# Performance work log

Hardware: AMD Instinct MI355X
Metric: run time of the kernel (lower is better)

Reference implementation:

```python
import jax, jax.numpy as jnp
import numpy as np


def _rotate_half(x):
    x1, x2 = jnp.split(x, 2, axis=-1)
    return jnp.concatenate((-x2, x1), axis=-1)


def setup_inputs() -> dict:
    key = jax.random.key(0)
    ks = jax.random.split(key, 8)
    B, T, C, H = 2, 2048, 1024, 16
    Dh = C // H
    x = jax.random.normal(ks[0], (B, T, C), dtype=jnp.float32)
    # RoPE tables (T, head_dim)
    inv_freq = 1.0 / (10000.0 ** (np.arange(0, Dh, 2, dtype=np.float32) / Dh))
    pos = np.arange(T, dtype=np.float32)
    freqs = np.einsum('t,f->tf', pos, inv_freq)
    emb = np.concatenate([freqs, freqs], axis=-1)
    cos = jnp.asarray(np.cos(emb), dtype=jnp.float32)
    sin = jnp.asarray(np.sin(emb), dtype=jnp.float32)
    # causal mask: 1 where attending allowed, 0 elsewhere
    mask = jnp.tril(jnp.ones((T, T), dtype=jnp.int32))
    s = 0.02
    Wq = jax.random.normal(ks[1], (C, C), dtype=jnp.float32) * s
    Wk = jax.random.normal(ks[2], (C, C), dtype=jnp.float32) * s
    Wv = jax.random.normal(ks[3], (C, C), dtype=jnp.float32) * s
    Wo = jax.random.normal(ks[4], (C, C), dtype=jnp.float32) * s
    return {"x": x, "cos": cos, "sin": sin, "mask": mask, "n_heads": H,
            "Wq": Wq, "Wk": Wk, "Wv": Wv, "Wo": Wo}


def reference(x, cos, sin, mask, n_heads, Wq, Wk, Wv, Wo):
    B, T, C = x.shape
    H = n_heads
    Dh = C // H
    scale = Dh ** (-0.5)
    # projections (torch Linear: x @ W.T), reshape to (B, H, T, Dh)
    def proj(W):
        return (x @ W.T).reshape(B, T, H, Dh).transpose(0, 2, 1, 3)
    q, k, v = proj(Wq), proj(Wk), proj(Wv)
    # RoPE: cos/sin broadcast as (1, 1, T, Dh)
    c = cos[None, None]
    s = sin[None, None]
    q = q * c + _rotate_half(q) * s
    k = k * c + _rotate_half(k) * s
    att = jnp.einsum('bhtd,bhsd->bhts', q, k) * scale
    att = jnp.where(mask == 0, -jnp.inf, att)
    att = jax.nn.softmax(att, axis=-1)
    out = jnp.einsum('bhts,bhsd->bhtd', att, v)
    out = out.transpose(0, 2, 1, 3).reshape(B, T, C)
    return out @ Wo.T
```

## Files before the change

kernel.cpp:

```cpp
#include <hip/hip_runtime.h>
#include <stdint.h>

#define B_   2
#define T_   2048
#define C_   1024
#define H_   16
#define BT   4096
#define KDIM 1024

typedef unsigned short u16;
typedef __attribute__((ext_vector_type(8))) __bf16 bf16v8;
typedef __attribute__((ext_vector_type(4))) float f32x4;
typedef __attribute__((ext_vector_type(16))) float f32x16;
typedef __attribute__((ext_vector_type(4))) unsigned int u32x4;
typedef __attribute__((ext_vector_type(2))) unsigned int u32x2;

#define MFMA16(a, b, c) __builtin_amdgcn_mfma_f32_16x16x32_bf16((a), (b), (c), 0, 0, 0)
#define MFMA32(a, b, c) __builtin_amdgcn_mfma_f32_32x32x16_bf16((a), (b), (c), 0, 0, 0)

#define BARRIER() do { asm volatile("" ::: "memory"); \
                       __builtin_amdgcn_s_barrier();  \
                       asm volatile("" ::: "memory"); } while (0)

__device__ __forceinline__ u16 f2bf(float f) {
  __bf16 h = (__bf16)f;
  union { __bf16 h; u16 u; } v; v.h = h;
  return v.u;
}
__device__ __forceinline__ float bf2f(u16 u) {
  union { uint32_t u; float f; } v; v.u = (uint32_t)u << 16;
  return v.f;
}

__device__ __forceinline__ void xhalf(uint32_t a, uint32_t b,
                                      uint32_t& lo, uint32_t& hi) {
#if defined(__has_builtin) && __has_builtin(__builtin_amdgcn_permlane32_swap)
  u32x2 r = __builtin_amdgcn_permlane32_swap(a, b, false, false);
  lo = r.x; hi = r.y;
#else
  const bool upper = (threadIdx.x & 32) != 0;
  lo = upper ? __shfl_xor(b, 32) : a;
  hi = upper ? b : __shfl_xor(a, 32);
#endif
}

__device__ __forceinline__ void gload16(const void* g, void* l) {
  __builtin_amdgcn_global_load_lds((__attribute__((address_space(1))) void*)g,
                                   (__attribute__((address_space(3))) void*)l,
                                   16, 0, 0);
}

__global__ __launch_bounds__(256) void cvt_f32_bf16(const float* __restrict__ in,
                                                    u16* __restrict__ out, int n) {
  int i = (blockIdx.x * 256 + threadIdx.x) * 4;
  if (i + 3 < n) {
    float4 v = *(const float4*)(in + i);
    ushort4 o;
    o.x = f2bf(v.x); o.y = f2bf(v.y); o.z = f2bf(v.z); o.w = f2bf(v.w);
    *(ushort4*)(out + i) = o;
  }
}

__global__ __launch_bounds__(256) void cvt_weights(
    const float* __restrict__ wq, const float* __restrict__ wk,
    const float* __restrict__ wv, const float* __restrict__ wo,
    u16* __restrict__ qkv_dst, u16* __restrict__ o_dst) {
  const int bid = blockIdx.x;
  const int sel = bid >> 10;
  const float* src = (sel == 0) ? wq : (sel == 1) ? wk : (sel == 2) ? wv : wo;
  u16* dst = (sel < 3) ? (qkv_dst + sel * 1048576) : o_dst;
  const int i = ((bid & 1023) * 256 + threadIdx.x) * 4;
  float4 v = *(const float4*)(src + i);
  ushort4 o;
  o.x = f2bf(v.x); o.y = f2bf(v.y); o.z = f2bf(v.z); o.w = f2bf(v.w);
  *(ushort4*)(dst + i) = o;
}

template<int EPI, int NN>
__global__ __launch_bounds__(256, 2) void gemm128(
    const u16* __restrict__ A, const u16* __restrict__ Bm,
    float* __restrict__ Cf,
    u16* __restrict__ qo, u16* __restrict__ ko, u16* __restrict__ vt,
    const float* __restrict__ cosT, const float* __restrict__ sinT)
{
  __shared__ __align__(16) u16 As[2][128 * 64];
  __shared__ __align__(16) u16 Bs[2][128 * 64];
  const int tid = threadIdx.x;
  const int lane = tid & 63;
  const int w = tid >> 6;
  const int wm = w >> 1, wn = w & 1;
  const int lmod = lane & 15, ldiv = lane >> 4;

  constexpr int NBX = NN / 128;
  constexpr int XG_BY = (NBX == 24) ? 8 : 4;
  constexpr int XG_BX = (NBX == 24) ? 12 : 8;
  const int x = blockIdx.x & 7;
  const int i = blockIdx.x >> 3;
  const int gy = (NBX == 24) ? (x >> 1) : x;
  const int gx = (NBX == 24) ? (x & 1) : 0;
  const int by = gy * XG_BY + (i % XG_BY);
  const int bx = gx * XG_BX + (i / XG_BY);
  const int row0 = by * 128, col0 = bx * 128;

  const int srow = tid >> 3;
  const int sswz = ((tid & 7) * 16) ^ ((srow & 7) << 4);
  const char* Abase = (const char*)A + (size_t)(row0 + srow) * (KDIM * 2) + sswz;
  const char* Bbase = (const char*)Bm + (size_t)(col0 + srow) * (KDIM * 2) + sswz;
  const int ldst = (tid & 192) * 16;

  auto stage = [&](int buf, int t) {
    const int kb = t * 128;
#pragma unroll
    for (int c = 0; c < 4; ++c)
      gload16(Abase + (size_t)c * 32 * (KDIM * 2) + kb,
              (char*)As[buf] + c * 4096 + ldst);
#pragma unroll
    for (int c = 0; c < 4; ++c)
      gload16(Bbase + (size_t)c * 32 * (KDIM * 2) + kb,
              (char*)Bs[buf] + c * 4096 + ldst);
  };

  f32x4 acc[4][4] = {};
  stage(0, 0);

  for (int t = 0; t < KDIM / 64; ++t) {
    const int cur = t & 1;
    BARRIER();
    if (t + 1 < KDIM / 64) {
      stage(cur ^ 1, t + 1);
      asm volatile("s_waitcnt vmcnt(8)" ::: "memory");
    } else {
      asm volatile("s_waitcnt vmcnt(0)" ::: "memory");
    }
    BARRIER();

    bf16v8 af[4][2], bfr[4][2];
#pragma unroll
    for (int mf = 0; mf < 4; ++mf) {
      const int rr = wm * 64 + mf * 16 + lmod;
#pragma unroll
      for (int kc = 0; kc < 2; ++kc)
        af[mf][kc] = *(const bf16v8*)((const char*)As[cur] + rr * 128 +
                          ((kc * 64 + ldiv * 16) ^ ((rr & 7) << 4)));
    }
#pragma unroll
    for (int nf = 0; nf < 4; ++nf) {
      const int rr = wn * 64 + nf * 16 + lmod;
#pragma unroll
      for (int kc = 0; kc < 2; ++kc)
        bfr[nf][kc] = *(const bf16v8*)((const char*)Bs[cur] + rr * 128 +
                          ((kc * 64 + ldiv * 16) ^ ((rr & 7) << 4)));
    }
#pragma unroll
    for (int kc = 0; kc < 2; ++kc)
#pragma unroll
      for (int mf = 0; mf < 4; ++mf)
#pragma unroll
        for (int nf = 0; nf < 4; ++nf)
          acc[mf][nf] = MFMA16(af[mf][kc], bfr[nf][kc], acc[mf][nf]);
  }

  if (EPI == 0) {
#pragma unroll
    for (int mf = 0; mf < 4; ++mf) {
      const int mbase = row0 + wm * 64 + mf * 16 + ldiv * 4;
#pragma unroll
      for (int nf = 0; nf < 4; ++nf) {
        const int n = col0 + wn * 64 + nf * 16 + lmod;
#pragma unroll
        for (int r = 0; r < 4; ++r)
          Cf[(size_t)(mbase + r) * NN + n] = acc[mf][nf][r];
      }
    }
  } else {
    const int nb = col0 + wn * 64;
    const int proj = nb >> 10;
    const int hh = (nb & 1023) >> 6;
    if (proj < 2) {
      u16* dst = proj ? ko : qo;
#pragma unroll
      for (int mf = 0; mf < 4; ++mf) {
#pragma unroll
        for (int r = 0; r < 4; ++r) {
          const int m = row0 + wm * 64 + mf * 16 + ldiv * 4 + r;
          const int b = m >> 11, t = m & 2047;
          u16* drow = dst + ((size_t)(b * H_ + hh) * T_ + t) * 64;
#pragma unroll
          for (int nf = 0; nf < 4; ++nf) {
            const int d = nf * 16 + lmod;
            const float cs = cosT[t * 64 + d];
            const float sn = sinT[t * 64 + d];
            const float other = (nf < 2) ? acc[mf][nf + 2][r] : acc[mf][nf - 2][r];
            float val = (nf < 2) ? (acc[mf][nf][r] * cs - other * sn)
                                 : (acc[mf][nf][r] * cs + other * sn);
            if (proj == 0) val *= 0.18033688011112042f;
            drow[d] = f2bf(val);
          }
        }
      }
    } else {
      BARRIER();
      char* scr = (char*)As + w * 8192;
#pragma unroll
      for (int nf = 0; nf < 4; ++nf)
#pragma unroll
        for (int mf = 0; mf < 4; ++mf)
#pragma unroll
          for (int rp = 0; rp < 2; ++rp) {
            const int dd = nf * 16 + lmod;
            const int t0 = mf * 16 + ldiv * 4 + rp * 2;
            const uint32_t pk = (uint32_t)f2bf(acc[mf][nf][rp * 2]) |
                                ((uint32_t)f2bf(acc[mf][nf][rp * 2 + 1]) << 16);
            *(uint32_t*)(scr + ((dd * 128 + t0 * 2) ^ ((dd & 7) << 4))) = pk;
          }
      __syncthreads();
      const int trow = row0 + wm * 64;
      const int bb = trow >> 11, tl = trow & 2047;
#pragma unroll
      for (int j = 0; j < 8; ++j) {
        const int dd = j * 8 + (lane >> 3);
        const int c = lane & 7;
        const u32x4 vv = *(const u32x4*)(scr + ((dd * 128 + c * 16) ^ ((dd & 7) << 4)));
        u16* drow = vt + ((size_t)((bb * H_ + hh) * 64 + dd)) * T_ + tl;
        *(u32x4*)((char*)drow + c * 16) = vv;
      }
    }
  }
}

__global__ __launch_bounds__(256, 2) void attn_fwd4(
    const u16* __restrict__ Q, const u16* __restrict__ K,
    const u16* __restrict__ Vt, u16* __restrict__ O,
    u16* __restrict__ part_o, float* __restrict__ pml)
{
  __shared__ __align__(16) u16 Kl[2][64 * 64];
  __shared__ __align__(16) u16 Vl[2][64 * 64];
  const int xcd = blockIdx.x & 7;
  const int i   = blockIdx.x >> 3;
  const int bh  = xcd * 4 + (i & 3);
  const int r   = i >> 2;
  int qb0, t0, t1, sid;
  if (r < 8) {
    qb0 = r * 128; t0 = 0; t1 = 2 * r + 2; sid = -1;
  } else {
    const int s = r - 8;
    const int c = 8 + (s >> 1);
    const int half = s & 1;
    qb0 = c * 128;
    t0 = half * (c + 1); t1 = t0 + (c + 1);
    sid = (bh * 8 + (c - 8)) * 2 + half;
  }

  const int tid = threadIdx.x, lane = tid & 63, w = tid >> 6;
  const int l31 = lane & 31, hi = lane >> 5;
  const int qrow = qb0 + w * 32;

  bf16v8 qf[4];
  {
    const u16* qp = Q + ((size_t)bh * T_ + qrow + l31) * 64 + hi * 8;
    qf[0] = *(const bf16v8*)(qp);
    qf[1] = *(const bf16v8*)(qp + 16);
    qf[2] = *(const bf16v8*)(qp + 32);
    qf[3] = *(const bf16v8*)(qp + 48);
  }

  float m2 = -1e30f, lsum = 0.f;
  f32x16 oacc0 = {}, oacc1 = {};

  const int scolb = (tid & 7) * 16;
  const int ldst = (tid & 192) * 16;

  auto stage = [&](int buf, int t) {
    const int s0 = t << 6;
#pragma unroll
    for (int c = 0; c < 2; ++c) {
      const int row = (c * 256 + tid) >> 3;
      const int sw = scolb ^ ((row & 7) << 4);
      gload16((const char*)(K + ((size_t)bh * T_ + s0 + row) * 64) + sw,
              (char*)Kl[buf] + c * 4096 + ldst);
    }
#pragma unroll
    for (int c = 0; c < 2; ++c) {
      const int row = (c * 256 + tid) >> 3;
      const int sw = scolb ^ ((row & 7) << 4);
      gload16((const char*)(Vt + ((size_t)(bh * 64 + row)) * T_ + s0) + sw,
              (char*)Vl[buf] + c * 4096 + ldst);
    }
  };

  auto substep = [&](int cur, int sub, int s0_sub) {
    bf16v8 kf[4], vf[4];
#pragma unroll
    for (int c = 0; c < 4; ++c) {
      const int row = sub * 32 + l31;
      kf[c] = *(const bf16v8*)((const char*)Kl[cur] + row * 128 +
                  ((c * 32 + hi * 16) ^ ((row & 7) << 4)));
    }
#pragma unroll
    for (int db = 0; db < 2; ++db)
#pragma unroll
      for (int kg = 0; kg < 2; ++kg) {
        const int row = db * 32 + l31;
        vf[db * 2 + kg] = *(const bf16v8*)((const char*)Vl[cur] + row * 128 +
                  ((sub * 64 + kg * 32 + hi * 16) ^ ((row & 7) << 4)));
      }
    f32x16 s = {};
    s = MFMA32(kf[0], qf[0], s);
    s = MFMA32(kf[1], qf[1], s);
    s = MFMA32(kf[2], qf[2], s);
    s = MFMA32(kf[3], qf[3], s);
    if (s0_sub + 31 > qrow) {
#pragma unroll
      for (int r2 = 0; r2 < 16; ++r2) {
        const int key = s0_sub + (r2 & 3) + 8 * (r2 >> 2) + 4 * hi;
        if (key > qrow + l31) s[r2] = -1e30f;
      }
    }
    float t8[8];
#pragma unroll
    for (int r2 = 0; r2 < 8; ++r2) t8[r2] = fmaxf(s[r2], s[r2 + 8]);
    float t4a = fmaxf(t8[0], t8[4]), t4b = fmaxf(t8[1], t8[5]);
    float t4c = fmaxf(t8[2], t8[6]), t4d = fmaxf(t8[3], t8[7]);
    float pmax = fmaxf(fmaxf(t4a, t4b), fmaxf(t4c, t4d));
    {
      uint32_t lo, hh2;
      xhalf(__builtin_bit_cast(uint32_t, pmax), __builtin_bit_cast(uint32_t, pmax), lo, hh2);
      pmax = fmaxf(__builtin_bit_cast(float, lo), __builtin_bit_cast(float, hh2));
    }
    if (!__all(pmax <= m2 + 11.5416f)) {
      const float mnew = fmaxf(m2, pmax);
      const float rs = __builtin_amdgcn_exp2f(m2 - mnew);
      lsum *= rs;
#pragma unroll
      for (int r2 = 0; r2 < 16; ++r2) { oacc0[r2] *= rs; oacc1[r2] *= rs; }
      m2 = mnew;
    }
    float p[16];
#pragma unroll
    for (int r2 = 0; r2 < 16; ++r2) p[r2] = __builtin_amdgcn_exp2f(s[r2] - m2);
    float a8[8];
#pragma unroll
    for (int r2 = 0; r2 < 8; ++r2) a8[r2] = p[r2] + p[r2 + 8];
    float a4a = a8[0] + a8[4], a4b = a8[1] + a8[5];
    float a4c = a8[2] + a8[6], a4d = a8[3] + a8[7];
    float ts = (a4a + a4b) + (a4c + a4d);
    {
      uint32_t lo, hh2;
      xhalf(__builtin_bit_cast(uint32_t, ts), __builtin_bit_cast(uint32_t, ts), lo, hh2);
      ts = __builtin_bit_cast(float, lo) + __builtin_bit_cast(float, hh2);
    }
    lsum += ts;
    uint32_t o[8];
#pragma unroll
    for (int jj = 0; jj < 8; ++jj) {
      const int r0 = 4 * (jj >> 1) + 2 * (jj & 1);
      uint32_t d;
      asm("v_cvt_pk_bf16_f32 %0, %1, %2" : "=v"(d) : "v"(p[r0]), "v"(p[r0 + 1]));
      o[jj] = d;
    }
#pragma unroll
    for (int kg = 0; kg < 2; ++kg) {
      uint32_t f0, f1, f2, f3;
      xhalf(o[4 * kg + 0], o[4 * kg + 2], f0, f2);
      xhalf(o[4 * kg + 1], o[4 * kg + 3], f1, f3);
      u32x4 fr;
      fr.x = f0; fr.y = f1; fr.z = f2; fr.w = f3;
      const bf16v8 pf = __builtin_bit_cast(bf16v8, fr);
      oacc0 = MFMA32(vf[kg], pf, oacc0);
      oacc1 = MFMA32(vf[2 + kg], pf, oacc1);
    }
  };

  stage(0, t0);
  for (int t = t0; t < t1; ++t) {
    const int cur = (t - t0) & 1;
    BARRIER();
    if (t + 1 < t1) {
      stage(cur ^ 1, t + 1);
      asm volatile("s_waitcnt vmcnt(8)" ::: "memory");
    } else {
      asm volatile("s_waitcnt vmcnt(0)" ::: "memory");
    }
    BARRIER();
#pragma unroll
    for (int sub = 0; sub < 2; ++sub) {
      const int s0_sub = t * 64 + sub * 32;
      if (s0_sub <= qrow + 31) substep(cur, sub, s0_sub);
    }
  }

  BARRIER();
  char* scr = (char*)Kl + w * 4096;
  const float inv = (sid < 0) ? (1.f / lsum) : 1.f;
#pragma unroll
  for (int r2 = 0; r2 < 8; ++r2) {
    const int r = r2 * 2;
    const int dd = (r & 3) + 8 * (r >> 2) + 4 * hi;
    const uint32_t pk0 = (uint32_t)f2bf(oacc0[r] * inv) |
                         ((uint32_t)f2bf(oacc0[r + 1] * inv) << 16);
    *(uint32_t*)(scr + ((l31 * 128 + dd * 2) ^ ((l31 & 7) << 4))) = pk0;
    const uint32_t pk1 = (uint32_t)f2bf(oacc1[r] * inv) |
                         ((uint32_t)f2bf(oacc1[r + 1] * inv) << 16);
    *(uint32_t*)(scr + ((l31 * 128 + (dd + 32) * 2) ^ ((l31 & 7) << 4))) = pk1;
  }
  __syncthreads();
  const int qq = lane >> 1, cc = lane & 1;
  if (sid < 0) {
    const int b = bh >> 4, hh = bh & 15;
    u16* orow = O + ((size_t)(b * T_ + qrow + qq)) * C_ + hh * 64 + cc * 32;
#pragma unroll
    for (int jj = 0; jj < 4; ++jj) {
      const u32x4 vv = *(const u32x4*)(scr + ((qq * 128 + cc * 64 + jj * 16) ^ ((qq & 7) << 4)));
      *(u32x4*)((char*)orow + jj * 16) = vv;
    }
  } else {
    u16* prow = part_o + ((size_t)(sid * 128 + w * 32 + qq)) * 64 + cc * 32;
#pragma unroll
    for (int jj = 0; jj < 4; ++jj) {
      const u32x4 vv = *(const u32x4*)(scr + ((qq * 128 + cc * 64 + jj * 16) ^ ((qq & 7) << 4)));
      *(u32x4*)((char*)prow + jj * 16) = vv;
    }
    if (lane < 32) {
      pml[sid * 256 + w * 32 + lane] = m2;
      pml[sid * 256 + 128 + w * 32 + lane] = lsum;
    }
  }
}

__global__ __launch_bounds__(256) void attn_combine(
    const u16* __restrict__ part_o, const float* __restrict__ pml,
    u16* __restrict__ O)
{
  const int combo = blockIdx.x;
  const int bh = combo >> 3, c8 = combo & 7;
  const int sid0 = (bh * 8 + c8) * 2;
  const int row = threadIdx.x >> 1, dh = threadIdx.x & 1;
  const float m0 = pml[sid0 * 256 + row];
  const float l0 = pml[sid0 * 256 + 128 + row];
  const float m1 = pml[(sid0 + 1) * 256 + row];
  const float l1 = pml[(sid0 + 1) * 256 + 128 + row];
  const float m = fmaxf(m0, m1);
  const float s0 = __builtin_amdgcn_exp2f(m0 - m);
  const float s1 = __builtin_amdgcn_exp2f(m1 - m);
  const float inv = 1.f / (l0 * s0 + l1 * s1);
  const u16* p0 = part_o + ((size_t)(sid0 * 128 + row)) * 64 + dh * 32;
  const u16* p1 = part_o + ((size_t)((sid0 + 1) * 128 + row)) * 64 + dh * 32;
  const int b = bh >> 4, hh = bh & 15;
  const int t = (8 + c8) * 128 + row;
  u16* dst = O + ((size_t)(b * T_ + t)) * C_ + hh * 64 + dh * 32;
#pragma unroll
  for (int j0 = 0; j0 < 4; ++j0) {
    const u32x4 a = *(const u32x4*)(p0 + j0 * 8);
    const u32x4 bq = *(const u32x4*)(p1 + j0 * 8);
    const u16* pa = (const u16*)&a;
    const u16* pb = (const u16*)&bq;
    u16 outv[8];
#pragma unroll
    for (int j = 0; j < 8; ++j)
      outv[j] = f2bf((bf2f(pa[j]) * s0 + bf2f(pb[j]) * s1) * inv);
    *(u32x4*)(dst + j0 * 8) = *(const u32x4*)outv;
  }
}

extern "C" void kernel_launch(void* const* d_in, const int* in_sizes, int n_in,
                              void* d_out, int out_size, void* d_ws, size_t ws_size,
                              hipStream_t stream) {
  const float* x    = (const float*)d_in[0];
  const float* cosT = (const float*)d_in[1];
  const float* sinT = (const float*)d_in[2];
  const float* Wq = (const float*)d_in[5];
  const float* Wk = (const float*)d_in[6];
  const float* Wv = (const float*)d_in[7];
  const float* Wo = (const float*)d_in[8];
  float* out = (float*)d_out;

  char* ws = (char*)d_ws;
  u16* xb   = (u16*)(ws);
  u16* wqkv = (u16*)(ws + 8388608);
  u16* wo   = (u16*)(ws + 14680064);
  u16* q    = (u16*)(ws + 16777216);
  u16* k    = (u16*)(ws + 25165824);
  u16* vt   = (u16*)(ws + 33554432);
  u16* aout = (u16*)(ws + 41943040);
  u16* part_o = xb;
  float* pml  = (float*)(ws + 8388608);

  cvt_f32_bf16<<<4096, 256, 0, stream>>>(x, xb, BT * C_);
  cvt_weights<<<4096, 256, 0, stream>>>(Wq, Wk, Wv, Wo, wqkv, wo);

  gemm128<1, 3072><<<768, 256, 0, stream>>>(xb, wqkv, nullptr,
                                            q, k, vt, cosT, sinT);
  attn_fwd4<<<768, 256, 0, stream>>>(q, k, vt, aout, part_o, pml);
  attn_combine<<<256, 256, 0, stream>>>(part_o, pml, aout);
  gemm128<0, 1024><<<256, 256, 0, stream>>>(aout, wo, out,
                                            nullptr, nullptr, nullptr,
                                            nullptr, nullptr);
}
```

Before: 116.1 us.

## Add dedicated QKV GEMM with 256x128 tiles and triple-buffered LDS pipeline

Replaces the templated 128x128 QKV projection GEMM with a dedicated 512-thread kernel that computes 256x128 tiles. The K loop uses a three-slot LDS ring with loads issued two iterations ahead, and MFMA phases are split in two and wrapped with s_setprio. This aims to hide global-load latency and to reuse each B tile across twice as many rows. In exchange it uses 144KB of LDS at one block per CU, with fewer blocks (384) and more barriers per iteration.

```diff
diff --git a/kernel.cpp b/kernel.cpp
--- a/kernel.cpp
+++ b/kernel.cpp
@@ -76,12 +76,150 @@
   *(ushort4*)(dst + i) = o;
 }
 
+__global__ __launch_bounds__(512, 1) void gemm_qkv(
+    const u16* __restrict__ A, const u16* __restrict__ Bm,
+    u16* __restrict__ qo, u16* __restrict__ ko, u16* __restrict__ vt,
+    const float* __restrict__ cosT, const float* __restrict__ sinT)
+{
+  constexpr int SLOT = 49152;
+  constexpr int ABYTES = 32768;
+  __shared__ __align__(16) char smem[3 * SLOT];
+  const int tid = threadIdx.x;
+  const int lane = tid & 63;
+  const int w = tid >> 6;
+  const int wm = w >> 1, wn = w & 1;
+  const int lmod = lane & 15, ldiv = lane >> 4;
+
+  const int x = blockIdx.x & 7;
+  const int i = blockIdx.x >> 3;
+  const int by = (x >> 1) * 4 + (i & 3);
+  const int bx = (x & 1) * 12 + (i >> 2);
+  const int row0 = by * 256, col0 = bx * 128;
+
+  const int ldst = (tid & 448) * 16;
+
+  auto stage_unit = [&](int k, int u) {
+    char* base = smem + (k % 3) * SLOT + ((u == 2) ? ABYTES : u * 16384);
+    const u16* src = (u == 2) ? Bm : A;
+    const int rbase = (u == 2) ? col0 : (row0 + u * 128);
+    const size_t koff = (size_t)k * 128;
+#pragma unroll
+    for (int c = 0; c < 2; ++c) {
+      const int row = c * 64 + (tid >> 3);
+      const int sw = ((tid & 7) * 16) ^ ((row & 7) << 4);
+      gload16((const char*)src + (size_t)(rbase + row) * 2048 + koff + sw,
+              base + c * 8192 + ldst);
+    }
+  };
+
+  f32x4 acc[4][4] = {};
+  stage_unit(0, 0); stage_unit(0, 1); stage_unit(0, 2);
+  stage_unit(1, 0); stage_unit(1, 1); stage_unit(1, 2);
+  asm volatile("s_waitcnt vmcnt(6)" ::: "memory");
+  BARRIER();
+
+  for (int kt = 0; kt < 16; ++kt) {
+    const char* buf = smem + (kt % 3) * SLOT;
+    bf16v8 bfr[4][2];
+#pragma unroll
+    for (int p = 0; p < 2; ++p) {
+      bf16v8 af[2][2];
+#pragma unroll
+      for (int ii = 0; ii < 2; ++ii) {
+        const int lr = wm * 64 + (p * 2 + ii) * 16 + lmod;
+#pragma unroll
+        for (int kc = 0; kc < 2; ++kc)
+          af[ii][kc] = *(const bf16v8*)(buf + lr * 128 +
+                            ((kc * 64 + ldiv * 16) ^ ((lr & 7) << 4)));
+      }
+      if (p == 0) {
+#pragma unroll
+        for (int nf = 0; nf < 4; ++nf) {
+          const int lr = wn * 64 + nf * 16 + lmod;
+#pragma unroll
+          for (int kc = 0; kc < 2; ++kc)
+            bfr[nf][kc] = *(const bf16v8*)(buf + ABYTES + lr * 128 +
+                              ((kc * 64 + ldiv * 16) ^ ((lr & 7) << 4)));
+        }
+        if (kt + 2 < 16) { stage_unit(kt + 2, 0); stage_unit(kt + 2, 1); }
+      } else {
+        if (kt + 2 < 16) stage_unit(kt + 2, 2);
+        if (kt <= 13)      { asm volatile("s_waitcnt vmcnt(6)" ::: "memory"); }
+        else if (kt == 14) { asm volatile("s_waitcnt vmcnt(0)" ::: "memory"); }
+      }
+      BARRIER();
+      __builtin_amdgcn_s_setprio(1);
+#pragma unroll
+      for (int ii = 0; ii < 2; ++ii)
+#pragma unroll
+        for (int nf = 0; nf < 4; ++nf)
+#pragma unroll
+          for (int kc = 0; kc < 2; ++kc)
+            acc[p * 2 + ii][nf] = MFMA16(af[ii][kc], bfr[nf][kc],
+                                         acc[p * 2 + ii][nf]);
+      __builtin_amdgcn_s_setprio(0);
+      BARRIER();
+    }
+  }
+
+  const int nb = col0 + wn * 64;
+  const int proj = nb >> 10;
+  const int hh = (nb & 1023) >> 6;
+  if (proj < 2) {
+    u16* dst = proj ? ko : qo;
+#pragma unroll
+    for (int mf = 0; mf < 4; ++mf) {
+#pragma unroll
+      for (int r = 0; r < 4; ++r) {
+        const int m = row0 + wm * 64 + mf * 16 + ldiv * 4 + r;
+        const int b = m >> 11, t = m & 2047;
+        u16* drow = dst + ((size_t)(b * H_ + hh) * T_ + t) * 64;
+#pragma unroll
+        for (int nf = 0; nf < 4; ++nf) {
+          const int d = nf * 16 + lmod;
+          const float cs = cosT[t * 64 + d];
+          const float sn = sinT[t * 64 + d];
+          const float other = (nf < 2) ? acc[mf][nf + 2][r] : acc[mf][nf - 2][r];
+          float val = (nf < 2) ? (acc[mf][nf][r] * cs - other * sn)
+                               : (acc[mf][nf][r] * cs + other * sn);
+          if (proj == 0) val *= 0.18033688011112042f;
+          drow[d] = f2bf(val);
+        }
+      }
+    }
+  } else {
+    BARRIER();
+    char* scr = smem + w * 8192;
+#pragma unroll
+    for (int nf = 0; nf < 4; ++nf)
+#pragma unroll
+      for (int mf = 0; mf < 4; ++mf)
+#pragma unroll
+        for (int rp = 0; rp < 2; ++rp) {
+          const int dd = nf * 16 + lmod;
+          const int t0 = mf * 16 + ldiv * 4 + rp * 2;
+          const uint32_t pk = (uint32_t)f2bf(acc[mf][nf][rp * 2]) |
+                              ((uint32_t)f2bf(acc[mf][nf][rp * 2 + 1]) << 16);
+          *(uint32_t*)(scr + ((dd * 128 + t0 * 2) ^ ((dd & 7) << 4))) = pk;
+        }
+    __syncthreads();
+    const int trow = row0 + wm * 64;
+    const int bb = trow >> 11, tl = trow & 2047;
+#pragma unroll
+    for (int j = 0; j < 8; ++j) {
+      const int dd = j * 8 + (lane >> 3);
+      const int c = lane & 7;
+      const u32x4 vv = *(const u32x4*)(scr + ((dd * 128 + c * 16) ^ ((dd & 7) << 4)));
+      u16* drow = vt + ((size_t)((bb * H_ + hh) * 64 + dd)) * T_ + tl;
+      *(u32x4*)((char*)drow + c * 16) = vv;
+    }
+  }
+}
+
 template<int EPI, int NN>
 __global__ __launch_bounds__(256, 2) void gemm128(
     const u16* __restrict__ A, const u16* __restrict__ Bm,
-    float* __restrict__ Cf,
-    u16* __restrict__ qo, u16* __restrict__ ko, u16* __restrict__ vt,
-    const float* __restrict__ cosT, const float* __restrict__ sinT)
+    float* __restrict__ Cf)
 {
   __shared__ __align__(16) u16 As[2][128 * 64];
   __shared__ __align__(16) u16 Bs[2][128 * 64];
@@ -92,15 +230,12 @@
   const int lmod = lane & 15, ldiv = lane >> 4;
 
   constexpr int NBX = NN / 128;
-  constexpr int XG_BY = (NBX == 24) ? 8 : 4;
-  constexpr int XG_BX = (NBX == 24) ? 12 : 8;
   const int x = blockIdx.x & 7;
   const int i = blockIdx.x >> 3;
-  const int gy = (NBX == 24) ? (x >> 1) : x;
-  const int gx = (NBX == 24) ? (x & 1) : 0;
-  const int by = gy * XG_BY + (i % XG_BY);
-  const int bx = gx * XG_BX + (i / XG_BY);
+  const int by = x * 4 + (i % 4);
+  const int bx = i / 4;
   const int row0 = by * 128, col0 = bx * 128;
+  (void)NBX;
 
   const int srow = tid >> 3;
   const int sswz = ((tid & 7) * 16) ^ ((srow & 7) << 4);
@@ -160,70 +295,15 @@
           acc[mf][nf] = MFMA16(af[mf][kc], bfr[nf][kc], acc[mf][nf]);
   }
 
-  if (EPI == 0) {
-#pragma unroll
-    for (int mf = 0; mf < 4; ++mf) {
-      const int mbase = row0 + wm * 64 + mf * 16 + ldiv * 4;
-#pragma unroll
-      for (int nf = 0; nf < 4; ++nf) {
-        const int n = col0 + wn * 64 + nf * 16 + lmod;
-#pragma unroll
-        for (int r = 0; r < 4; ++r)
-          Cf[(size_t)(mbase + r) * NN + n] = acc[mf][nf][r];
-      }
-    }
-  } else {
-    const int nb = col0 + wn * 64;
-    const int proj = nb >> 10;
-    const int hh = (nb & 1023) >> 6;
-    if (proj < 2) {
-      u16* dst = proj ? ko : qo;
-#pragma unroll
-      for (int mf = 0; mf < 4; ++mf) {
-#pragma unroll
-        for (int r = 0; r < 4; ++r) {
-          const int m = row0 + wm * 64 + mf * 16 + ldiv * 4 + r;
-          const int b = m >> 11, t = m & 2047;
-          u16* drow = dst + ((size_t)(b * H_ + hh) * T_ + t) * 64;
-#pragma unroll
-          for (int nf = 0; nf < 4; ++nf) {
-            const int d = nf * 16 + lmod;
-            const float cs = cosT[t * 64 + d];
-            const float sn = sinT[t * 64 + d];
-            const float other = (nf < 2) ? acc[mf][nf + 2][r] : acc[mf][nf - 2][r];
-            float val = (nf < 2) ? (acc[mf][nf][r] * cs - other * sn)
-                                 : (acc[mf][nf][r] * cs + other * sn);
-            if (proj == 0) val *= 0.18033688011112042f;
-            drow[d] = f2bf(val);
-          }
-        }
-      }
-    } else {
-      BARRIER();
-      char* scr = (char*)As + w * 8192;
-#pragma unroll
-      for (int nf = 0; nf < 4; ++nf)
-#pragma unroll
-        for (int mf = 0; mf < 4; ++mf)
-#pragma unroll
-          for (int rp = 0; rp < 2; ++rp) {
-            const int dd = nf * 16 + lmod;
-            const int t0 = mf * 16 + ldiv * 4 + rp * 2;
-            const uint32_t pk = (uint32_t)f2bf(acc[mf][nf][rp * 2]) |
-                                ((uint32_t)f2bf(acc[mf][nf][rp * 2 + 1]) << 16);
-            *(uint32_t*)(scr + ((dd * 128 + t0 * 2) ^ ((dd & 7) << 4))) = pk;
-          }
-      __syncthreads();
-      const int trow = row0 + wm * 64;
-      const int bb = trow >> 11, tl = trow & 2047;
-#pragma unroll
-      for (int j = 0; j < 8; ++j) {
-        const int dd = j * 8 + (lane >> 3);
-        const int c = lane & 7;
-        const u32x4 vv = *(const u32x4*)(scr + ((dd * 128 + c * 16) ^ ((dd & 7) << 4)));
-        u16* drow = vt + ((size_t)((bb * H_ + hh) * 64 + dd)) * T_ + tl;
-        *(u32x4*)((char*)drow + c * 16) = vv;
-      }
+#pragma unroll
+  for (int mf = 0; mf < 4; ++mf) {
+    const int mbase = row0 + wm * 64 + mf * 16 + ldiv * 4;
+#pragma unroll
+    for (int nf = 0; nf < 4; ++nf) {
+      const int n = col0 + wn * 64 + nf * 16 + lmod;
+#pragma unroll
+      for (int r = 0; r < 4; ++r)
+        Cf[(size_t)(mbase + r) * NN + n] = acc[mf][nf][r];
     }
   }
 }
@@ -488,11 +568,8 @@
   cvt_f32_bf16<<<4096, 256, 0, stream>>>(x, xb, BT * C_);
   cvt_weights<<<4096, 256, 0, stream>>>(Wq, Wk, Wv, Wo, wqkv, wo);
 
-  gemm128<1, 3072><<<768, 256, 0, stream>>>(xb, wqkv, nullptr,
-                                            q, k, vt, cosT, sinT);
+  gemm_qkv<<<384, 512, 0, stream>>>(xb, wqkv, q, k, vt, cosT, sinT);
   attn_fwd4<<<768, 256, 0, stream>>>(q, k, vt, aout, part_o, pml);
   attn_combine<<<256, 256, 0, stream>>>(part_o, pml, aout);
-  gemm128<0, 1024><<<256, 256, 0, stream>>>(aout, wo, out,
-                                            nullptr, nullptr, nullptr,
-                                            nullptr, nullptr);
-}
+  gemm128<0, 1024><<<256, 256, 0, stream>>>(aout, wo, out);
+}
```

After: 117.5 us. No clear change (+1.2%).
